# Kernel tuning notes

Measured on AMD Instinct MI355X. Metric: run time of the kernel, lower is better.

The kernel has to match this reference:

```python
import jax, jax.numpy as jnp
import numpy as np

BITS = 8
NUM_HEADS = 16
EMB = 1024
MLP = 4096
BATCH = 4
SEQ = 1024


def _fq(x, bits, signed=True, narrow=False):
    """Fake-quantize with per-tensor absmax scale (brevitas MinMax/MaxStats style),
    straight-through-estimator round. signed+narrow => weight quant; signed non-narrow
    => activation quant; unsigned => QuantReLU output."""
    if signed:
        qmax = 2.0 ** (bits - 1) - 1.0
        qmin = -qmax if narrow else -(qmax + 1.0)
    else:
        qmax = 2.0 ** bits - 1.0
        qmin = 0.0
    scale = jax.lax.stop_gradient(jnp.max(jnp.abs(x)) / qmax)
    scale = jnp.maximum(scale, jnp.asarray(1e-8, x.dtype))
    q = x / scale
    q = q + jax.lax.stop_gradient(jnp.round(q) - q)  # STE round
    return jnp.clip(q, qmin, qmax) * scale


def _layernorm(x, eps=1e-5):
    mu = jnp.mean(x, axis=-1, keepdims=True)
    var = jnp.mean(jnp.square(x - mu), axis=-1, keepdims=True)
    return (x - mu) * jax.lax.rsqrt(var + eps)


def setup_inputs() -> dict:
    key = jax.random.key(0)
    ks = jax.random.split(key, 11)
    def w(k, shape, fan_in):
        return jax.random.normal(k, shape, jnp.float32) * (1.0 / np.sqrt(fan_in))
    return {
        "x": jax.random.normal(ks[0], (BATCH, SEQ, EMB), jnp.float32),
        "Wq": w(ks[1], (EMB, EMB), EMB), "bq": jnp.zeros((EMB,), jnp.float32),
        "Wk": w(ks[2], (EMB, EMB), EMB), "bk": jnp.zeros((EMB,), jnp.float32),
        "Wv": w(ks[3], (EMB, EMB), EMB), "bv": jnp.zeros((EMB,), jnp.float32),
        "Wo": w(ks[4], (EMB, EMB), EMB), "bo": jnp.zeros((EMB,), jnp.float32),
        "W1": w(ks[5], (MLP, EMB), EMB), "b1": jnp.zeros((MLP,), jnp.float32),
        "W2": w(ks[6], (EMB, MLP), MLP), "b2": jnp.zeros((EMB,), jnp.float32),
    }


def reference(x, Wq, bq, Wk, bk, Wv, bv, Wo, bo, W1, b1, W2, b2):
    B, S, E = x.shape
    H, D = NUM_HEADS, EMB // NUM_HEADS
    fqw = lambda W: _fq(W, BITS, signed=True, narrow=True)   # weight quant
    fqb = lambda b: _fq(b, BITS, signed=True)                # bias quant
    fqa = lambda a: _fq(a, BITS, signed=True)                # act quant

    # sdp_input_quant
    qx = fqa(x)
    # separate (unpacked) in-projections, torch Linear: y = x @ W.T + b
    q = qx @ fqw(Wq).T + fqb(bq)
    k = qx @ fqw(Wk).T + fqb(bk)
    v = qx @ fqw(Wv).T + fqb(bv)
    # [B,H,S,D]
    q = q.reshape(B, S, H, D).transpose(0, 2, 1, 3)
    k = k.reshape(B, S, H, D).transpose(0, 2, 1, 3)
    v = v.reshape(B, S, H, D).transpose(0, 2, 1, 3)

    q_scaled = fqa(q * (1.0 / np.sqrt(D)))          # q_scaled_quant
    k_t = fqa(k.transpose(0, 1, 3, 2))              # k_transposed_quant
    v = fqa(v)                                      # v_quant

    scores = jnp.einsum('bhqd,bhdk->bhqk', q_scaled, k_t)
    scores = fqa(scores)                            # softmax_input_quant
    attn = jax.nn.softmax(scores, axis=-1)
    attn = fqa(attn)                                # attn_output_weights_quant

    ctx = jnp.einsum('bhqk,bhkd->bhqd', attn, v)
    ctx = ctx.transpose(0, 2, 1, 3).reshape(B, S, E)
    ctx = fqa(ctx)                                  # out_proj_input_quant
    attn_out = ctx @ fqw(Wo).T + fqb(bo)

    # residual_sdp (QuantEltwiseAdd input quant on both operands) + layer-norm
    h = _layernorm(fqa(x) + fqa(attn_out))

    # MLP: QuantIdentity -> QuantLinear -> QuantReLU(unsigned) -> QuantLinear
    m = fqa(h)
    m = m @ fqw(W1).T + fqb(b1)
    m = _fq(jax.nn.relu(m), BITS, signed=False)
    m = m @ fqw(W2).T + fqb(b2)

    return _layernorm(fqa(h) + fqa(m))
```

## Files before the change

kernel.cpp:

```cpp
#include <hip/hip_runtime.h>
#include <cstdint>
#include <cstddef>

#define TB_B 4
#define TB_S 1024
#define TB_E 1024
#define TB_H 16
#define TB_D 64
#define TB_MLP 4096
#define TB_ROWS (TB_B * TB_S)

typedef int int4v __attribute__((ext_vector_type(4)));

#define LGKM0() __asm__ volatile("s_waitcnt lgkmcnt(0)" ::: "memory")
#define CMEMBAR() __asm__ volatile("" ::: "memory")
#define RAW_BARRIER() do { __asm__ volatile("" ::: "memory"); \
  __builtin_amdgcn_s_barrier(); __asm__ volatile("" ::: "memory"); } while (0)

static __device__ __forceinline__ void atomicMaxF(float* addr, float v) {
  atomicMax(reinterpret_cast<unsigned int*>(addr), __float_as_uint(v));
}

static __device__ __forceinline__ float fast_exp2(float x) {
#if __has_builtin(__builtin_amdgcn_exp2f)
  return __builtin_amdgcn_exp2f(x);
#else
  return exp2f(x);
#endif
}

static __device__ __forceinline__ void gl2lds16(const void* g, void* l) {
  __builtin_amdgcn_global_load_lds(
      (const __attribute__((address_space(1))) void*)g,
      (__attribute__((address_space(3))) void*)l, 16, 0, 0);
}

struct AMDesc { const float* p; long n4; int slot; };
struct AMBatch { AMDesc d[13]; };
__global__ __launch_bounds__(256) void absmax_multi_kernel(AMBatch bt, float* ws) {
  AMDesc d = bt.d[blockIdx.y];
  float m = 0.f;
  long stride = (long)gridDim.x * 256;
  for (long i = (long)blockIdx.x * 256 + threadIdx.x; i < d.n4; i += stride) {
    float4 v = ((const float4*)d.p)[i];
    m = fmaxf(m, fmaxf(fmaxf(fabsf(v.x), fabsf(v.y)), fmaxf(fabsf(v.z), fabsf(v.w))));
  }
#pragma unroll
  for (int o = 32; o; o >>= 1) m = fmaxf(m, __shfl_down(m, o, 64));
  __shared__ float sm[4];
  if (!(threadIdx.x & 63)) sm[threadIdx.x >> 6] = m;
  __syncthreads();
  if (threadIdx.x == 0)
    atomicMaxF(ws + d.slot, fmaxf(fmaxf(sm[0], sm[1]), fmaxf(sm[2], sm[3])));
}

struct QMDesc { const float* in; signed char* out; long n4; int slot; float qmin; };
struct QMBatch { QMDesc d[7]; };
__global__ __launch_bounds__(256) void quant8_multi_kernel(QMBatch bt, const float* ws) {
  QMDesc d = bt.d[blockIdx.y];
  float scale = fmaxf(ws[d.slot] / 127.f, 1e-8f);
  long stride = (long)gridDim.x * 256;
  for (long i = (long)blockIdx.x * 256 + threadIdx.x; i < d.n4; i += stride) {
    float4 v = ((const float4*)d.in)[i];
    char4 o;
    o.x = (signed char)(int)fminf(fmaxf(rintf(v.x / scale), d.qmin), 127.f);
    o.y = (signed char)(int)fminf(fmaxf(rintf(v.y / scale), d.qmin), 127.f);
    o.z = (signed char)(int)fminf(fmaxf(rintf(v.z / scale), d.qmin), 127.f);
    o.w = (signed char)(int)fminf(fmaxf(rintf(v.w / scale), d.qmin), 127.f);
    ((char4*)d.out)[i] = o;
  }
}

struct BDesc { const float* in; float* out; int n4; int slot; };
struct BBatch { BDesc d[6]; };
__global__ __launch_bounds__(256) void bias_quant_multi_kernel(BBatch bt, const float* ws) {
  BDesc d = bt.d[blockIdx.y];
  float scale = fmaxf(ws[d.slot] / 127.f, 1e-8f);
  int i = blockIdx.x * 256 + threadIdx.x;
  if (i < d.n4) {
    float4 v = ((const float4*)d.in)[i];
    float4 o;
    o.x = fminf(fmaxf(rintf(v.x / scale), -128.f), 127.f) * scale;
    o.y = fminf(fmaxf(rintf(v.y / scale), -128.f), 127.f) * scale;
    o.z = fminf(fmaxf(rintf(v.z / scale), -128.f), 127.f) * scale;
    o.w = fminf(fmaxf(rintf(v.w / scale), -128.f), 127.f) * scale;
    ((float4*)d.out)[i] = o;
  }
}

__global__ __launch_bounds__(256) void quant8_kernel(const float* __restrict__ in,
                                                     signed char* __restrict__ out8, long n4,
                                                     const float* __restrict__ amax_p,
                                                     float pre, float qmin) {
  float scale = fmaxf(amax_p[0] * pre / 127.f, 1e-8f);
  long stride = (long)gridDim.x * 256;
  for (long i = (long)blockIdx.x * 256 + threadIdx.x; i < n4; i += stride) {
    float4 v = ((const float4*)in)[i];
    char4 o;
    o.x = (signed char)(int)fminf(fmaxf(rintf(v.x * pre / scale), qmin), 127.f);
    o.y = (signed char)(int)fminf(fmaxf(rintf(v.y * pre / scale), qmin), 127.f);
    o.z = (signed char)(int)fminf(fmaxf(rintf(v.z * pre / scale), qmin), 127.f);
    o.w = (signed char)(int)fminf(fmaxf(rintf(v.w * pre / scale), qmin), 127.f);
    ((char4*)out8)[i] = o;
  }
}

__global__ __launch_bounds__(256) void relu_quant8_kernel(const float* __restrict__ in,
                                                          signed char* __restrict__ out8, long n4,
                                                          const float* __restrict__ amax_p) {
  float scale = fmaxf(amax_p[0] / 255.f, 1e-8f);
  long stride = (long)gridDim.x * 256;
  for (long i = (long)blockIdx.x * 256 + threadIdx.x; i < n4; i += stride) {
    float4 v = ((const float4*)in)[i];
    char4 o;
    o.x = (signed char)((int)fminf(fmaxf(rintf(fmaxf(v.x, 0.f) / scale), 0.f), 255.f) - 128);
    o.y = (signed char)((int)fminf(fmaxf(rintf(fmaxf(v.y, 0.f) / scale), 0.f), 255.f) - 128);
    o.z = (signed char)((int)fminf(fmaxf(rintf(fmaxf(v.z, 0.f) / scale), 0.f), 255.f) - 128);
    o.w = (signed char)((int)fminf(fmaxf(rintf(fmaxf(v.w, 0.f) / scale), 0.f), 255.f) - 128);
    ((char4*)out8)[i] = o;
  }
}

__global__ __launch_bounds__(256) void rowsum_i8_kernel(const signed char* __restrict__ w8,
                                                        int* __restrict__ out, int Kdim) {
  const int row = blockIdx.x, t = threadIdx.x;
  const signed char* p = w8 + (long)row * Kdim;
  int s = 0;
  for (int i = t * 16; i < Kdim; i += 4096) {
    int4v v = *(const int4v*)(p + i);
    const signed char* b = (const signed char*)&v;
#pragma unroll
    for (int j = 0; j < 16; j++) s += b[j];
  }
#pragma unroll
  for (int o = 32; o; o >>= 1) s += __shfl_down(s, o, 64);
  __shared__ int sm[4];
  if (!(t & 63)) sm[t >> 6] = s;
  __syncthreads();
  if (t == 0) out[row] = sm[0] + sm[1] + sm[2] + sm[3];
}

__global__ __launch_bounds__(512, 2) void gemm_i8_kernel(
    const signed char* __restrict__ A, const signed char* __restrict__ Bw,
    const float* __restrict__ biasq,
    const float* __restrict__ amax_a, float div_a,
    const float* __restrict__ amax_b,
    const int* __restrict__ rowsum,
    float* __restrict__ C, int M, int N, int K,
    float* __restrict__ amax_out, int relu_amax, int mode) {
  __shared__ signed char Asm[4][8192];
  __shared__ signed char Bsm[4][8192];
  __shared__ float redm[8];
  const int t = threadIdx.x;
  int bx, by;
  {
    int lin = blockIdx.y * gridDim.x + blockIdx.x;
    if ((gridDim.y & 7) == 0) {
      int xcd = lin & 7, j = lin >> 3;
      bx = j % gridDim.x;
      by = (gridDim.y >> 3) * xcd + j / gridDim.x;
    } else { bx = blockIdx.x; by = blockIdx.y; }
  }
  const int m0 = by * 128, n0 = bx * 128;
  const int w = t >> 6, lane = t & 63;
  const int fr = lane & 15, quad = lane >> 4;
  const int wm = w >> 1, wn = w & 1;
  const int r0 = t >> 2;
  const int csrc = (((t & 3) ^ ((t >> 3) & 3)) << 4);
  const int sx = ((quad ^ ((fr >> 1) & 3)) << 4);

  int4v acc[2][4];
#pragma unroll
  for (int r = 0; r < 2; r++)
#pragma unroll
    for (int c = 0; c < 4; c++) acc[r][c] = (int4v){0, 0, 0, 0};

  const long arow = (long)(m0 + r0) * K + csrc;
  const long brow = (long)(n0 + r0) * K + csrc;

  auto stage = [&](int buf, int kt) {
    const int kk = kt << 6;
    gl2lds16(A + arow + kk, Asm[buf] + t * 16);
    gl2lds16(Bw + brow + kk, Bsm[buf] + t * 16);
  };
  auto compute = [&](int buf) {
    int4v af[2], bf[4];
#pragma unroll
    for (int r = 0; r < 2; r++)
      af[r] = *(const int4v*)(Asm[buf] + (wm * 32 + r * 16 + fr) * 64 + sx);
#pragma unroll
    for (int c = 0; c < 4; c++)
      bf[c] = *(const int4v*)(Bsm[buf] + (wn * 64 + c * 16 + fr) * 64 + sx);
#pragma unroll
    for (int r = 0; r < 2; r++)
#pragma unroll
      for (int c = 0; c < 4; c++)
        acc[r][c] = __builtin_amdgcn_mfma_i32_16x16x64_i8(af[r], bf[c], acc[r][c], 0, 0, 0);
  };

  const int nt = K >> 6;
  stage(0, 0);
  stage(1, 1);
  stage(2, 2);
  for (int kt = 0; kt < nt; ++kt) {
    const int rem = nt - 1 - kt;
    if (rem >= 2)      { __asm__ volatile("s_waitcnt vmcnt(4)" ::: "memory"); }
    else if (rem == 1) { __asm__ volatile("s_waitcnt vmcnt(2)" ::: "memory"); }
    else               { __asm__ volatile("s_waitcnt vmcnt(0)" ::: "memory"); }
    RAW_BARRIER();
    if (kt + 3 < nt) stage((kt + 3) & 3, kt + 3);
    compute(kt & 3);
  }

  const int seg = (mode == 1) ? (n0 >> 10) : 0;
  const float s_a = fmaxf(amax_a[0] / div_a, 1e-8f);
  const float s_b = fmaxf(amax_b[seg] / 127.f, 1e-8f);
  const float s = s_a * s_b;
  float lmax = 0.f;
#pragma unroll
  for (int r = 0; r < 2; r++) {
    int rbase = m0 + wm * 32 + r * 16 + quad * 4;
#pragma unroll
    for (int c = 0; c < 4; c++) {
      int col = n0 + wn * 64 + c * 16 + fr;
      int corr = rowsum ? (rowsum[col] << 7) : 0;
      float bi = biasq[col];
      if (mode == 1) {
        int h = (col >> 6) & 15, dd = col & 63;
        float* cbase = C + (long)seg * ((long)TB_ROWS * TB_E);
#pragma unroll
        for (int g = 0; g < 4; g++) {
          int m = rbase + g;
          int b = m >> 10, sdx = m & 1023;
          float o = (float)acc[r][c][g] * s + bi;
          lmax = fmaxf(lmax, fabsf(o));
          cbase[((((long)b * TB_H + h) * TB_S) + sdx) * TB_D + dd] = o;
        }
      } else {
#pragma unroll
        for (int g = 0; g < 4; g++) {
          float o = (float)(acc[r][c][g] + corr) * s + bi;
          lmax = fmaxf(lmax, relu_amax ? fmaxf(o, 0.f) : fabsf(o));
          C[(long)(rbase + g) * N + col] = o;
        }
      }
    }
  }
#pragma unroll
  for (int o = 32; o; o >>= 1) lmax = fmaxf(lmax, __shfl_down(lmax, o, 64));
  if (!lane) redm[w] = lmax;
  __syncthreads();
  if (t == 0) {
    float m01 = fmaxf(fmaxf(redm[0], redm[1]), fmaxf(redm[2], redm[3]));
    float m23 = fmaxf(fmaxf(redm[4], redm[5]), fmaxf(redm[6], redm[7]));
    atomicMaxF(amax_out + seg, fmaxf(m01, m23));
  }
}

__global__ __launch_bounds__(256) void quant8_vb_kernel(const float* __restrict__ v,
                                                        const float* __restrict__ amax_p,
                                                        signed char* __restrict__ v8b) {
  __shared__ signed char tile[64][80];
  const int bh = blockIdx.x;
  const int jb = blockIdx.y;
  const int s0 = jb * 64;
  const int t = threadIdx.x;
  const float scale = fmaxf(amax_p[0] / 127.f, 1e-8f);
#pragma unroll
  for (int it = 0; it < 4; it++) {
    int idx = t + it * 256;
    int r = idx >> 4, c4 = (idx & 15) * 4;
    float4 vv = *(const float4*)(v + ((long)bh * TB_S + s0 + r) * TB_D + c4);
    tile[c4 + 0][r] = (signed char)(int)fminf(fmaxf(rintf(vv.x / scale), -128.f), 127.f);
    tile[c4 + 1][r] = (signed char)(int)fminf(fmaxf(rintf(vv.y / scale), -128.f), 127.f);
    tile[c4 + 2][r] = (signed char)(int)fminf(fmaxf(rintf(vv.z / scale), -128.f), 127.f);
    tile[c4 + 3][r] = (signed char)(int)fminf(fmaxf(rintf(vv.w / scale), -128.f), 127.f);
  }
  __syncthreads();
  int d = t >> 2, sb = (t & 3) * 16;
  int4v o = *(const int4v*)&tile[d][sb];
  *(int4v*)(v8b + (((long)bh * 16 + jb) * 64 + d) * 64 + sb) = o;
}

__global__ __launch_bounds__(256) void attn_rowmax_kernel(const signed char* __restrict__ q8,
                                                          const signed char* __restrict__ k8,
                                                          int* __restrict__ irowmax,
                                                          int* __restrict__ imax_out) {
  const int bh = blockIdx.x;
  const int t = threadIdx.x, w = t >> 6, lane = t & 63;
  const int fr = lane & 15, quad = lane >> 4;
  const int i0 = blockIdx.y * 64 + w * 16;
  const long base = (long)bh * TB_S;
  int4v qf = *(const int4v*)(q8 + (base + i0 + fr) * 64 + quad * 16);
  int mx = -2147483647, mn = 2147483647;
  for (int j0 = 0; j0 < TB_S; j0 += 16) {
    int4v kf = *(const int4v*)(k8 + (base + j0 + fr) * 64 + quad * 16);
    int4v sc = __builtin_amdgcn_mfma_i32_16x16x64_i8(kf, qf, (int4v){0, 0, 0, 0}, 0, 0, 0);
    mx = max(mx, max(max(sc[0], sc[1]), max(sc[2], sc[3])));
    mn = min(mn, min(min(sc[0], sc[1]), min(sc[2], sc[3])));
  }
  mx = max(mx, __shfl_xor(mx, 16, 64));
  mx = max(mx, __shfl_xor(mx, 32, 64));
  mn = min(mn, __shfl_xor(mn, 16, 64));
  mn = min(mn, __shfl_xor(mn, 32, 64));
  if (quad == 0) irowmax[(long)bh * TB_S + i0 + fr] = mx;
  int gm = max(mx, -mn);
#pragma unroll
  for (int o = 32; o; o >>= 1) gm = max(gm, __shfl_down(gm, o, 64));
  __shared__ int sm[4];
  if (!lane) sm[w] = gm;
  __syncthreads();
  if (t == 0) atomicMax(imax_out, max(max(sm[0], sm[1]), max(sm[2], sm[3])));
}

__global__ __launch_bounds__(256) void attn_rowsum_kernel(
    const signed char* __restrict__ q8, const signed char* __restrict__ k8,
    const int* __restrict__ irowmax, const int* __restrict__ imax_p,
    const float* __restrict__ amax_q, const float* __restrict__ amax_k,
    float* __restrict__ rowl, float* __restrict__ amax_attn) {
  const int bh = blockIdx.x;
  const int t = threadIdx.x, w = t >> 6, lane = t & 63;
  const int fr = lane & 15, quad = lane >> 4;
  const int i0 = blockIdx.y * 64 + w * 16;
  const float s_q = fmaxf(amax_q[0] * 0.125f / 127.f, 1e-8f);
  const float s_k = fmaxf(amax_k[0] / 127.f, 1e-8f);
  const float sqk = s_q * s_k;
  const float s_sc = fmaxf((float)imax_p[0] * sqk / 127.f, 1e-8f);
  const float c1 = sqk / s_sc;
  const float aa = s_sc * 1.44269504088896340736f;
  const long base = (long)bh * TB_S;
  int4v qf = *(const int4v*)(q8 + (base + i0 + fr) * 64 + quad * 16);
  const int imr = irowmax[base + i0 + fr];
  const float qmax = fminf(fmaxf(rintf((float)imr * c1), -128.f), 127.f);
  const float qa = qmax * aa;
  float l = 0.f;
  for (int j0 = 0; j0 < TB_S; j0 += 16) {
    int4v kf = *(const int4v*)(k8 + (base + j0 + fr) * 64 + quad * 16);
    int4v sc = __builtin_amdgcn_mfma_i32_16x16x64_i8(kf, qf, (int4v){0, 0, 0, 0}, 0, 0, 0);
#pragma unroll
    for (int g = 0; g < 4; g++) {
      float qv = rintf((float)sc[g] * c1);
      l += fast_exp2(fmaf(qv, aa, -qa));
    }
  }
  l += __shfl_xor(l, 16, 64);
  l += __shfl_xor(l, 32, 64);
  if (quad == 0) rowl[base + i0 + fr] = l;
  float inv = 1.f / l;
#pragma unroll
  for (int o = 32; o; o >>= 1) inv = fmaxf(inv, __shfl_down(inv, o, 64));
  __shared__ float smf[4];
  if (!lane) smf[w] = inv;
  __syncthreads();
  if (t == 0) atomicMaxF(amax_attn, fmaxf(fmaxf(smf[0], smf[1]), fmaxf(smf[2], smf[3])));
}

__global__ __launch_bounds__(256) void attn_pv_kernel(
    const signed char* __restrict__ q8, const signed char* __restrict__ k8,
    const signed char* __restrict__ v8b,
    const int* __restrict__ irowmax, const int* __restrict__ imax_p,
    const float* __restrict__ amax_q, const float* __restrict__ amax_k,
    const float* __restrict__ amax_v, const float* __restrict__ amax_attn,
    const float* __restrict__ rowl,
    float* __restrict__ ctx, float* __restrict__ amax_ctx) {
  __shared__ signed char latt[4][16][80];
  const int bh = blockIdx.x, b = bh >> 4, h = bh & 15;
  const int t = threadIdx.x, w = t >> 6, lane = t & 63;
  const int fr = lane & 15, quad = lane >> 4;
  const int i0 = blockIdx.y * 64 + w * 16;
  const float s_q = fmaxf(amax_q[0] * 0.125f / 127.f, 1e-8f);
  const float s_k = fmaxf(amax_k[0] / 127.f, 1e-8f);
  const float sqk = s_q * s_k;
  const float s_sc = fmaxf((float)imax_p[0] * sqk / 127.f, 1e-8f);
  const float c1 = sqk / s_sc;
  const float aa = s_sc * 1.44269504088896340736f;
  const float s_v = fmaxf(amax_v[0] / 127.f, 1e-8f);
  const float s_at = fmaxf(amax_attn[0] / 127.f, 1e-8f);
  const long base = (long)bh * TB_S;
  int4v qf = *(const int4v*)(q8 + (base + i0 + fr) * 64 + quad * 16);
  const int imr = irowmax[base + i0 + fr];
  const float qmax = fminf(fmaxf(rintf((float)imr * c1), -128.f), 127.f);
  const float bexp = qmax * aa;
  const float li = rowl[base + i0 + fr];
  const float invls = 1.f / (li * s_at);
  int4v accv[4];
#pragma unroll
  for (int dtile = 0; dtile < 4; dtile++) accv[dtile] = (int4v){0, 0, 0, 0};

  for (int j0 = 0; j0 < TB_S; j0 += 64) {
#pragma unroll
    for (int tt = 0; tt < 4; tt++) {
      int4v kf = *(const int4v*)(k8 + (base + j0 + tt * 16 + fr) * 64 + quad * 16);
      int4v sc = __builtin_amdgcn_mfma_i32_16x16x64_i8(kf, qf, (int4v){0, 0, 0, 0}, 0, 0, 0);
      int packed = 0;
#pragma unroll
      for (int g = 0; g < 4; g++) {
        float qv = rintf((float)sc[g] * c1);
        float e = fast_exp2(fmaf(qv, aa, -bexp));
        float f = fmaf(e, invls, 12582912.f);
        packed |= (__float_as_int(f) & 255) << (g * 8);
      }
      *(int*)&latt[w][fr][tt * 16 + quad * 4] = packed;
    }
    LGKM0();
    int4v af = *(const int4v*)&latt[w][fr][quad * 16];
    const signed char* vbase = v8b + (((long)bh * 16 + (j0 >> 6)) * 64) * 64;
#pragma unroll
    for (int dtile = 0; dtile < 4; dtile++) {
      int4v vf = *(const int4v*)(vbase + (dtile * 16 + fr) * 64 + quad * 16);
      accv[dtile] = __builtin_amdgcn_mfma_i32_16x16x64_i8(af, vf, accv[dtile], 0, 0, 0);
    }
    CMEMBAR();
  }
  const float sav = s_at * s_v;
  float cmax = 0.f;
#pragma unroll
  for (int dtile = 0; dtile < 4; dtile++) {
#pragma unroll
    for (int g = 0; g < 4; g++) {
      float val = (float)accv[dtile][g] * sav;
      cmax = fmaxf(cmax, fabsf(val));
      int irow = i0 + quad * 4 + g;
      ctx[(((long)(b * TB_S + irow)) * TB_H + h) * TB_D + dtile * 16 + fr] = val;
    }
  }
#pragma unroll
  for (int o = 32; o; o >>= 1) cmax = fmaxf(cmax, __shfl_down(cmax, o, 64));
  __shared__ float smf[4];
  if (!lane) smf[w] = cmax;
  __syncthreads();
  if (t == 0) atomicMaxF(amax_ctx, fmaxf(fmaxf(smf[0], smf[1]), fmaxf(smf[2], smf[3])));
}

__global__ __launch_bounds__(256) void resid_ln_kernel(const signed char* __restrict__ a8,
                                                       const float* __restrict__ amax_a,
                                                       const float* __restrict__ braw,
                                                       const float* __restrict__ amax_b,
                                                       float* __restrict__ outp,
                                                       float* __restrict__ amax_out) {
  const int t = threadIdx.x, w = t >> 6, lane = t & 63;
  const int row = blockIdx.x * 4 + w;
  const float sa = fmaxf(amax_a[0] / 127.f, 1e-8f);
  const float sb = fmaxf(amax_b[0] / 127.f, 1e-8f);
  const long base = (long)row * TB_E;
  float v[16];
  float s = 0.f, q = 0.f;
#pragma unroll
  for (int j = 0; j < 4; j++) {
    char4 a = ((const char4*)(a8 + base))[j * 64 + lane];
    float4 bv = *(const float4*)(braw + base + j * 256 + lane * 4);
    float x0 = (float)a.x * sa + fminf(fmaxf(rintf(bv.x / sb), -128.f), 127.f) * sb;
    float x1 = (float)a.y * sa + fminf(fmaxf(rintf(bv.y / sb), -128.f), 127.f) * sb;
    float x2 = (float)a.z * sa + fminf(fmaxf(rintf(bv.z / sb), -128.f), 127.f) * sb;
    float x3 = (float)a.w * sa + fminf(fmaxf(rintf(bv.w / sb), -128.f), 127.f) * sb;
    v[j * 4 + 0] = x0; v[j * 4 + 1] = x1; v[j * 4 + 2] = x2; v[j * 4 + 3] = x3;
    s += (x0 + x1) + (x2 + x3);
    q += (x0 * x0 + x1 * x1) + (x2 * x2 + x3 * x3);
  }
#pragma unroll
  for (int o = 32; o; o >>= 1) {
    s += __shfl_xor(s, o, 64);
    q += __shfl_xor(q, o, 64);
  }
  const float mu = s * (1.f / TB_E);
  const float var = fmaxf(q * (1.f / TB_E) - mu * mu, 0.f);
  const float rs = 1.f / sqrtf(var + 1e-5f);
  float lm = 0.f;
#pragma unroll
  for (int j = 0; j < 4; j++) {
    float4 o4;
    o4.x = (v[j * 4 + 0] - mu) * rs;
    o4.y = (v[j * 4 + 1] - mu) * rs;
    o4.z = (v[j * 4 + 2] - mu) * rs;
    o4.w = (v[j * 4 + 3] - mu) * rs;
    *(float4*)(outp + base + j * 256 + lane * 4) = o4;
    lm = fmaxf(lm, fmaxf(fmaxf(fabsf(o4.x), fabsf(o4.y)), fmaxf(fabsf(o4.z), fabsf(o4.w))));
  }
#pragma unroll
  for (int o = 32; o; o >>= 1) lm = fmaxf(lm, __shfl_down(lm, o, 64));
  __shared__ float redm[4];
  if (!lane) redm[w] = lm;
  __syncthreads();
  if (t == 0) atomicMaxF(amax_out, fmaxf(fmaxf(redm[0], redm[1]), fmaxf(redm[2], redm[3])));
}

#define SL_X 0
#define SL_WQ 1
#define SL_WK 2
#define SL_WV 3
#define SL_WO 4
#define SL_W1 5
#define SL_W2 6
#define SL_BQ 7
#define SL_BK 8
#define SL_BV 9
#define SL_BO 10
#define SL_B1 11
#define SL_B2 12
#define SL_Q 13
#define SL_K 14
#define SL_V 15
#define SL_SCI 16
#define SL_ATTN 17
#define SL_CTX 18
#define SL_AO 19
#define SL_H 20
#define SL_RELU 21
#define SL_M2 22
#define SL_DUMMY 23

static inline int nblocks(long n) {
  long b = (n + 255) / 256;
  return (int)(b > 2048 ? 2048 : b);
}

extern "C" void kernel_launch(void* const* d_in, const int* in_sizes, int n_in,
                              void* d_out, int out_size, void* d_ws, size_t ws_size,
                              hipStream_t stream) {
  const float* x  = (const float*)d_in[0];
  const float* Wq = (const float*)d_in[1];
  const float* bq = (const float*)d_in[2];
  const float* Wk = (const float*)d_in[3];
  const float* bk = (const float*)d_in[4];
  const float* Wv = (const float*)d_in[5];
  const float* bv = (const float*)d_in[6];
  const float* Wo = (const float*)d_in[7];
  const float* bo = (const float*)d_in[8];
  const float* W1 = (const float*)d_in[9];
  const float* b1 = (const float*)d_in[10];
  const float* W2 = (const float*)d_in[11];
  const float* b2 = (const float*)d_in[12];
  float* ws = (float*)d_ws;
  float* out = (float*)d_out;

  const long SZ_XE = (long)TB_ROWS * TB_E;
  const long SZ_W  = (long)TB_E * TB_E;
  const long SZ_M1 = (long)TB_ROWS * TB_MLP;

  const long OFF_QBQ = 1024, OFF_QBK = 2048, OFF_QBV = 3072, OFF_QBO = 4096;
  const long OFF_QB1 = 5120, OFF_QB2 = 9216;
  const long OFF_RSUM = 10240;
  const long OFF_Q  = 65536;
  const long OFF_K  = OFF_Q + SZ_XE;
  const long OFF_V  = OFF_K + SZ_XE;
  const long OFF_M2 = OFF_V + SZ_XE;
  const long OFF_IRM = OFF_M2 + SZ_XE;
  const long OFF_ROWL = OFF_IRM + 65536;
  const long OFF_M1 = OFF_ROWL + 65536;
  const long OFF_I8 = OFF_M1 + SZ_M1;

  float* qbuf = ws + OFF_Q;  float* kbuf = ws + OFF_K;  float* vbuf = ws + OFF_V;
  float* m2   = ws + OFF_M2;
  int*   irowmax = (int*)(ws + OFF_IRM);
  float* rowl = ws + OFF_ROWL;
  float* m1 = ws + OFF_M1;
  float* ctx = qbuf;
  float* attn_out = kbuf;
  float* hbuf = vbuf;
  float* qbq_ = ws + OFF_QBQ; float* qbk_ = ws + OFF_QBK;
  float* qbv_ = ws + OFF_QBV; float* qbo_ = ws + OFF_QBO;
  float* qb1_ = ws + OFF_QB1; float* qb2_ = ws + OFF_QB2;
  int* rsum = (int*)(ws + OFF_RSUM);
  int* imax = (int*)(ws + SL_SCI);

  signed char* i8base = (signed char*)(ws + OFF_I8);
  signed char* qx8  = i8base;
  signed char* wq8  = qx8 + SZ_XE;
  signed char* wk8  = wq8 + SZ_W;
  signed char* wv8  = wk8 + SZ_W;
  signed char* wo8  = wv8 + SZ_W;
  signed char* w18  = wo8 + SZ_W;
  signed char* w28  = w18 + SZ_XE;
  signed char* ctx8 = w28 + SZ_XE;
  signed char* m08  = ctx8 + SZ_XE;
  signed char* m18  = m08 + SZ_XE;
  signed char* q8   = m18 + SZ_M1;
  signed char* k8   = q8 + SZ_XE;
  signed char* v8b  = k8 + SZ_XE;

  hipMemsetAsync(ws, 0, 4096, stream);

  AMBatch am;
  am.d[0]  = {x,  SZ_XE/4, SL_X};
  am.d[1]  = {Wq, SZ_W/4,  SL_WQ};
  am.d[2]  = {Wk, SZ_W/4,  SL_WK};
  am.d[3]  = {Wv, SZ_W/4,  SL_WV};
  am.d[4]  = {Wo, SZ_W/4,  SL_WO};
  am.d[5]  = {W1, SZ_XE/4, SL_W1};
  am.d[6]  = {W2, SZ_XE/4, SL_W2};
  am.d[7]  = {bq, 256,     SL_BQ};
  am.d[8]  = {bk, 256,     SL_BK};
  am.d[9]  = {bv, 256,     SL_BV};
  am.d[10] = {bo, 256,     SL_BO};
  am.d[11] = {b1, 1024,    SL_B1};
  am.d[12] = {b2, 256,     SL_B2};
  absmax_multi_kernel<<<dim3(64, 13), 256, 0, stream>>>(am, ws);

  QMBatch qm;
  qm.d[0] = {x,  qx8, SZ_XE/4, SL_X,  -128.f};
  qm.d[1] = {Wq, wq8, SZ_W/4,  SL_WQ, -127.f};
  qm.d[2] = {Wk, wk8, SZ_W/4,  SL_WK, -127.f};
  qm.d[3] = {Wv, wv8, SZ_W/4,  SL_WV, -127.f};
  qm.d[4] = {W1, w18, SZ_XE/4, SL_W1, -127.f};
  qm.d[5] = {W2, w28, SZ_XE/4, SL_W2, -127.f};
  qm.d[6] = {Wo, wo8, SZ_W/4,  SL_WO, -127.f};
  quant8_multi_kernel<<<dim3(64, 7), 256, 0, stream>>>(qm, ws);
  rowsum_i8_kernel<<<TB_E, 256, 0, stream>>>(w28, rsum, TB_MLP);
  BBatch bb;
  bb.d[0] = {bq, qbq_, 256,  SL_BQ};
  bb.d[1] = {bk, qbk_, 256,  SL_BK};
  bb.d[2] = {bv, qbv_, 256,  SL_BV};
  bb.d[3] = {bo, qbo_, 256,  SL_BO};
  bb.d[4] = {b1, qb1_, 1024, SL_B1};
  bb.d[5] = {b2, qb2_, 256,  SL_B2};
  bias_quant_multi_kernel<<<dim3(4, 6), 256, 0, stream>>>(bb, ws);

  gemm_i8_kernel<<<dim3(3*TB_E/128, TB_ROWS/128), 512, 0, stream>>>(
      qx8, wq8, qbq_, ws + SL_X, 127.f, ws + SL_WQ, nullptr, qbuf,
      TB_ROWS, 3*TB_E, TB_E, ws + SL_Q, 0, 1);

  quant8_kernel<<<2048, 256, 0, stream>>>(qbuf, q8, SZ_XE/4, ws + SL_Q, 0.125f, -128.f);
  quant8_kernel<<<2048, 256, 0, stream>>>(kbuf, k8, SZ_XE/4, ws + SL_K, 1.f, -128.f);
  quant8_vb_kernel<<<dim3(TB_B*TB_H, TB_S/64), 256, 0, stream>>>(vbuf, ws + SL_V, v8b);

  attn_rowmax_kernel<<<dim3(TB_B*TB_H, TB_S/64), 256, 0, stream>>>(q8, k8, irowmax, imax);
  attn_rowsum_kernel<<<dim3(TB_B*TB_H, TB_S/64), 256, 0, stream>>>(
      q8, k8, irowmax, imax, ws + SL_Q, ws + SL_K, rowl, ws + SL_ATTN);
  attn_pv_kernel<<<dim3(TB_B*TB_H, TB_S/64), 256, 0, stream>>>(
      q8, k8, v8b, irowmax, imax, ws + SL_Q, ws + SL_K, ws + SL_V, ws + SL_ATTN,
      rowl, ctx, ws + SL_CTX);

  quant8_kernel<<<2048, 256, 0, stream>>>(ctx, ctx8, SZ_XE/4, ws + SL_CTX, 1.f, -128.f);
  gemm_i8_kernel<<<dim3(TB_E/128, TB_ROWS/128), 512, 0, stream>>>(
      ctx8, wo8, qbo_, ws + SL_CTX, 127.f, ws + SL_WO, nullptr, attn_out,
      TB_ROWS, TB_E, TB_E, ws + SL_AO, 0, 0);

  resid_ln_kernel<<<TB_ROWS/4, 256, 0, stream>>>(qx8, ws + SL_X, attn_out, ws + SL_AO, hbuf, ws + SL_H);

  quant8_kernel<<<2048, 256, 0, stream>>>(hbuf, m08, SZ_XE/4, ws + SL_H, 1.f, -128.f);
  gemm_i8_kernel<<<dim3(TB_MLP/128, TB_ROWS/128), 512, 0, stream>>>(
      m08, w18, qb1_, ws + SL_H, 127.f, ws + SL_W1, nullptr, m1,
      TB_ROWS, TB_MLP, TB_E, ws + SL_RELU, 1, 0);
  relu_quant8_kernel<<<nblocks(SZ_M1/4), 256, 0, stream>>>(m1, m18, SZ_M1/4, ws + SL_RELU);
  gemm_i8_kernel<<<dim3(TB_E/128, TB_ROWS/128), 512, 0, stream>>>(
      m18, w28, qb2_, ws + SL_RELU, 255.f, ws + SL_W2, rsum, m2,
      TB_ROWS, TB_E, TB_MLP, ws + SL_M2, 0, 0);

  resid_ln_kernel<<<TB_ROWS/4, 256, 0, stream>>>(m08, ws + SL_H, m2, ws + SL_M2, out, ws + SL_DUMMY);
}
```

Baseline: 468.8 us.

## Shrink int8 GEMM tiles to 64x64 and double-buffer attention PV staging

The int8 GEMM moves from 128x128 tiles with 512 threads to 64x64 tiles with 256 threads, with smaller LDS buffers and a higher occupancy hint. This gives more blocks per launch for better CU fill, at the cost of less operand reuse per tile. Separately, the attention PV kernel now double-buffers its LDS staging of probabilities, computing the next QK tile into registers while the current PV MFMAs run. This is meant to overlap the QK/exp work with the PV matmul.

Result: slower. 525.7 us (+12.1%).

```diff
diff --git a/kernel.cpp b/kernel.cpp
--- a/kernel.cpp
+++ b/kernel.cpp
@@ -140,7 +140,7 @@
   if (t == 0) out[row] = sm[0] + sm[1] + sm[2] + sm[3];
 }
 
-__global__ __launch_bounds__(512, 2) void gemm_i8_kernel(
+__global__ __launch_bounds__(256, 4) void gemm_i8_kernel(
     const signed char* __restrict__ A, const signed char* __restrict__ Bw,
     const float* __restrict__ biasq,
     const float* __restrict__ amax_a, float div_a,
@@ -148,9 +148,9 @@
     const int* __restrict__ rowsum,
     float* __restrict__ C, int M, int N, int K,
     float* __restrict__ amax_out, int relu_amax, int mode) {
-  __shared__ signed char Asm[4][8192];
-  __shared__ signed char Bsm[4][8192];
-  __shared__ float redm[8];
+  __shared__ signed char Asm[4][4096];
+  __shared__ signed char Bsm[4][4096];
+  __shared__ float redm[4];
   const int t = threadIdx.x;
   int bx, by;
   {
@@ -161,7 +161,7 @@
       by = (gridDim.y >> 3) * xcd + j / gridDim.x;
     } else { bx = blockIdx.x; by = blockIdx.y; }
   }
-  const int m0 = by * 128, n0 = bx * 128;
+  const int m0 = by * 64, n0 = bx * 64;
   const int w = t >> 6, lane = t & 63;
   const int fr = lane & 15, quad = lane >> 4;
   const int wm = w >> 1, wn = w & 1;
@@ -169,11 +169,11 @@
   const int csrc = (((t & 3) ^ ((t >> 3) & 3)) << 4);
   const int sx = ((quad ^ ((fr >> 1) & 3)) << 4);
 
-  int4v acc[2][4];
+  int4v acc[2][2];
 #pragma unroll
   for (int r = 0; r < 2; r++)
 #pragma unroll
-    for (int c = 0; c < 4; c++) acc[r][c] = (int4v){0, 0, 0, 0};
+    for (int c = 0; c < 2; c++) acc[r][c] = (int4v){0, 0, 0, 0};
 
   const long arow = (long)(m0 + r0) * K + csrc;
   const long brow = (long)(n0 + r0) * K + csrc;
@@ -184,17 +184,17 @@
     gl2lds16(Bw + brow + kk, Bsm[buf] + t * 16);
   };
   auto compute = [&](int buf) {
-    int4v af[2], bf[4];
+    int4v af[2], bf[2];
 #pragma unroll
     for (int r = 0; r < 2; r++)
       af[r] = *(const int4v*)(Asm[buf] + (wm * 32 + r * 16 + fr) * 64 + sx);
 #pragma unroll
-    for (int c = 0; c < 4; c++)
-      bf[c] = *(const int4v*)(Bsm[buf] + (wn * 64 + c * 16 + fr) * 64 + sx);
+    for (int c = 0; c < 2; c++)
+      bf[c] = *(const int4v*)(Bsm[buf] + (wn * 32 + c * 16 + fr) * 64 + sx);
 #pragma unroll
     for (int r = 0; r < 2; r++)
 #pragma unroll
-      for (int c = 0; c < 4; c++)
+      for (int c = 0; c < 2; c++)
         acc[r][c] = __builtin_amdgcn_mfma_i32_16x16x64_i8(af[r], bf[c], acc[r][c], 0, 0, 0);
   };
 
@@ -221,8 +221,8 @@
   for (int r = 0; r < 2; r++) {
     int rbase = m0 + wm * 32 + r * 16 + quad * 4;
 #pragma unroll
-    for (int c = 0; c < 4; c++) {
-      int col = n0 + wn * 64 + c * 16 + fr;
+    for (int c = 0; c < 2; c++) {
+      int col = n0 + wn * 32 + c * 16 + fr;
       int corr = rowsum ? (rowsum[col] << 7) : 0;
       float bi = biasq[col];
       if (mode == 1) {
@@ -250,11 +250,8 @@
   for (int o = 32; o; o >>= 1) lmax = fmaxf(lmax, __shfl_down(lmax, o, 64));
   if (!lane) redm[w] = lmax;
   __syncthreads();
-  if (t == 0) {
-    float m01 = fmaxf(fmaxf(redm[0], redm[1]), fmaxf(redm[2], redm[3]));
-    float m23 = fmaxf(fmaxf(redm[4], redm[5]), fmaxf(redm[6], redm[7]));
-    atomicMaxF(amax_out + seg, fmaxf(m01, m23));
-  }
+  if (t == 0)
+    atomicMaxF(amax_out + seg, fmaxf(fmaxf(redm[0], redm[1]), fmaxf(redm[2], redm[3])));
 }
 
 __global__ __launch_bounds__(256) void quant8_vb_kernel(const float* __restrict__ v,
@@ -363,7 +360,7 @@
     const float* __restrict__ amax_v, const float* __restrict__ amax_attn,
     const float* __restrict__ rowl,
     float* __restrict__ ctx, float* __restrict__ amax_ctx) {
-  __shared__ signed char latt[4][16][80];
+  __shared__ signed char latt[2][4][16][80];
   const int bh = blockIdx.x, b = bh >> 4, h = bh & 15;
   const int t = threadIdx.x, w = t >> 6, lane = t & 63;
   const int fr = lane & 15, quad = lane >> 4;
@@ -387,7 +384,8 @@
 #pragma unroll
   for (int dtile = 0; dtile < 4; dtile++) accv[dtile] = (int4v){0, 0, 0, 0};
 
-  for (int j0 = 0; j0 < TB_S; j0 += 64) {
+  int pk[4];
+  auto qk4 = [&](int j0) {
 #pragma unroll
     for (int tt = 0; tt < 4; tt++) {
       int4v kf = *(const int4v*)(k8 + (base + j0 + tt * 16 + fr) * 64 + quad * 16);
@@ -400,17 +398,33 @@
         float f = fmaf(e, invls, 12582912.f);
         packed |= (__float_as_int(f) & 255) << (g * 8);
       }
-      *(int*)&latt[w][fr][tt * 16 + quad * 4] = packed;
+      pk[tt] = packed;
     }
+  };
+
+  qk4(0);
+#pragma unroll
+  for (int tt = 0; tt < 4; tt++)
+    *(int*)&latt[0][w][fr][tt * 16 + quad * 4] = pk[tt];
+
+  const int njt = TB_S / 64;
+  for (int jt = 0; jt < njt; ++jt) {
+    const int cur = jt & 1;
+    if (jt + 1 < njt) qk4((jt + 1) * 64);
     LGKM0();
-    int4v af = *(const int4v*)&latt[w][fr][quad * 16];
-    const signed char* vbase = v8b + (((long)bh * 16 + (j0 >> 6)) * 64) * 64;
+    int4v af = *(const int4v*)&latt[cur][w][fr][quad * 16];
+    const signed char* vbase = v8b + (((long)bh * 16 + jt) * 64) * 64;
 #pragma unroll
     for (int dtile = 0; dtile < 4; dtile++) {
       int4v vf = *(const int4v*)(vbase + (dtile * 16 + fr) * 64 + quad * 16);
       accv[dtile] = __builtin_amdgcn_mfma_i32_16x16x64_i8(af, vf, accv[dtile], 0, 0, 0);
     }
-    CMEMBAR();
+    if (jt + 1 < njt) {
+      CMEMBAR();
+#pragma unroll
+      for (int tt = 0; tt < 4; tt++)
+        *(int*)&latt[cur ^ 1][w][fr][tt * 16 + quad * 4] = pk[tt];
+    }
   }
   const float sav = s_at * s_v;
   float cmax = 0.f;
@@ -615,7 +629,7 @@
   bb.d[5] = {b2, qb2_, 256,  SL_B2};
   bias_quant_multi_kernel<<<dim3(4, 6), 256, 0, stream>>>(bb, ws);
 
-  gemm_i8_kernel<<<dim3(3*TB_E/128, TB_ROWS/128), 512, 0, stream>>>(
+  gemm_i8_kernel<<<dim3(3*TB_E/64, TB_ROWS/64), 256, 0, stream>>>(
       qx8, wq8, qbq_, ws + SL_X, 127.f, ws + SL_WQ, nullptr, qbuf,
       TB_ROWS, 3*TB_E, TB_E, ws + SL_Q, 0, 1);
 
@@ -631,18 +645,18 @@
       rowl, ctx, ws + SL_CTX);
 
   quant8_kernel<<<2048, 256, 0, stream>>>(ctx, ctx8, SZ_XE/4, ws + SL_CTX, 1.f, -128.f);
-  gemm_i8_kernel<<<dim3(TB_E/128, TB_ROWS/128), 512, 0, stream>>>(
+  gemm_i8_kernel<<<dim3(TB_E/64, TB_ROWS/64), 256, 0, stream>>>(
       ctx8, wo8, qbo_, ws + SL_CTX, 127.f, ws + SL_WO, nullptr, attn_out,
       TB_ROWS, TB_E, TB_E, ws + SL_AO, 0, 0);
 
   resid_ln_kernel<<<TB_ROWS/4, 256, 0, stream>>>(qx8, ws + SL_X, attn_out, ws + SL_AO, hbuf, ws + SL_H);
 
   quant8_kernel<<<2048, 256, 0, stream>>>(hbuf, m08, SZ_XE/4, ws + SL_H, 1.f, -128.f);
-  gemm_i8_kernel<<<dim3(TB_MLP/128, TB_ROWS/128), 512, 0, stream>>>(
+  gemm_i8_kernel<<<dim3(TB_MLP/64, TB_ROWS/64), 256, 0, stream>>>(
       m08, w18, qb1_, ws + SL_H, 127.f, ws + SL_W1, nullptr, m1,
       TB_ROWS, TB_MLP, TB_E, ws + SL_RELU, 1, 0);
   relu_quant8_kernel<<<nblocks(SZ_M1/4), 256, 0, stream>>>(m1, m18, SZ_M1/4, ws + SL_RELU);
-  gemm_i8_kernel<<<dim3(TB_E/128, TB_ROWS/128), 512, 0, stream>>>(
+  gemm_i8_kernel<<<dim3(TB_E/64, TB_ROWS/64), 256, 0, stream>>>(
       m18, w28, qb2_, ws + SL_RELU, 255.f, ws + SL_W2, rsum, m2,
       TB_ROWS, TB_E, TB_MLP, ws + SL_M2, 0, 0);
 
```
